# Optimization experiments

Measured on AMD Instinct MI355X. Metric: run time of the kernel, lower is better.

## Reference

```python
import jax, jax.numpy as jnp
import numpy as np

HID = 64      # RNN hidden size (fixed in source)
K = 3         # B-spline order (pykan default)
NUM = 5       # grid intervals (pykan default)
DIMS = [64, 16, 1]  # layer_nums_small_nobi


def make_grid(in_dim):
    # uniform grid on [-1,1] extended by K knots each side -> NUM+2K+1 = 12 knots
    h = 2.0 / NUM
    g = jnp.arange(-K, NUM + K + 1, dtype=jnp.float32) * h - 1.0
    return jnp.broadcast_to(g, (in_dim, g.shape[0]))


def bspline_basis(x, grid):
    # x: (b, in), grid: (in, G) -> basis (b, in, G-K-1) via Cox-de Boor
    xe = x[..., None]
    B = ((xe >= grid[:, :-1]) & (xe < grid[:, 1:])).astype(x.dtype)
    for d in range(1, K + 1):
        left = (xe - grid[:, :-(d + 1)]) / (grid[:, d:-1] - grid[:, :-(d + 1)]) * B[..., :-1]
        right = (grid[:, d + 1:] - xe) / (grid[:, d + 1:] - grid[:, 1:-d]) * B[..., 1:]
        B = left + right
    return B  # (b, in, NUM+K)


def kan_layer(x, grid, coef, sb, sp):
    # coef: (in, out, NUM+K); sb, sp: (in, out)
    bas = bspline_basis(x, grid)                      # (b, in, NUM+K)
    spl = jnp.einsum('bik,iok->bio', bas, coef)       # per-edge spline value
    return jnp.einsum('bi,io->bo', jax.nn.silu(x), sb) + jnp.einsum('bio,io->bo', spl, sp)


def rnn_layer(x, w_ih, w_hh, b_ih, b_hh, return_seq):
    # x: (b, t, f), tanh RNN, h0 = 0
    h0 = jnp.zeros((x.shape[0], HID), x.dtype)
    def step(h, xt):
        h = jnp.tanh(xt @ w_ih.T + h @ w_hh.T + b_ih + b_hh)
        return h, (h if return_seq else 0.0)
    hT, ys = jax.lax.scan(step, h0, jnp.swapaxes(x, 0, 1))
    return jnp.swapaxes(ys, 0, 1) if return_seq else hT


def setup_inputs() -> dict:
    key = jax.random.key(0)
    ks = jax.random.split(key, 16)
    Bsz, T, F = 2048, 256, 64
    s = 1.0 / np.sqrt(HID)
    inp = {'x': jax.random.normal(ks[0], (Bsz, T, F), jnp.float32)}
    inp['w_ih0'] = jax.random.uniform(ks[1], (HID, F), jnp.float32, -s, s)
    inp['w_hh0'] = jax.random.uniform(ks[2], (HID, HID), jnp.float32, -s, s)
    inp['b_ih0'] = jax.random.uniform(ks[3], (HID,), jnp.float32, -s, s)
    inp['b_hh0'] = jax.random.uniform(ks[4], (HID,), jnp.float32, -s, s)
    inp['w_ih1'] = jax.random.uniform(ks[5], (HID, HID), jnp.float32, -s, s)
    inp['w_hh1'] = jax.random.uniform(ks[6], (HID, HID), jnp.float32, -s, s)
    inp['b_ih1'] = jax.random.uniform(ks[7], (HID,), jnp.float32, -s, s)
    inp['b_hh1'] = jax.random.uniform(ks[8], (HID,), jnp.float32, -s, s)
    kk = 9
    for i, (di, do) in enumerate(zip(DIMS[:-1], DIMS[1:])):
        inp[f'grid{i}'] = make_grid(di)
        inp[f'coef{i}'] = 0.1 * jax.random.normal(ks[kk], (di, do, NUM + K), jnp.float32)
        inp[f'sb{i}'] = (1.0 / np.sqrt(di)) * jnp.ones((di, do), jnp.float32) + 0.05 * jax.random.normal(ks[kk + 1], (di, do), jnp.float32)
        inp[f'sp{i}'] = jnp.ones((di, do), jnp.float32)
        kk += 2
    return inp


def reference(x, w_ih0, w_hh0, b_ih0, b_hh0, w_ih1, w_hh1, b_ih1, b_hh1,
              grid0, coef0, sb0, sp0, grid1, coef1, sb1, sp1):
    h1 = rnn_layer(x, w_ih0, w_hh0, b_ih0, b_hh0, return_seq=True)   # (b,t,64)
    out = rnn_layer(h1, w_ih1, w_hh1, b_ih1, b_hh1, return_seq=False)  # last step only
    out = kan_layer(out, grid0, coef0, sb0, sp0)   # (b,16)
    out = kan_layer(out, grid1, coef1, sb1, sp1)   # (b,1)
    return jnp.squeeze(jax.nn.sigmoid(out), 1)     # (b,)
```

## Files before the change

kernel.cpp:

```cpp
#include <hip/hip_runtime.h>
#include <cstdint>
#include <cstddef>

typedef __attribute__((ext_vector_type(8))) __bf16 bf16x8;
typedef __attribute__((ext_vector_type(4))) float f32x4;

#define MFMA16(a, b, c) __builtin_amdgcn_mfma_f32_16x16x32_bf16((a), (b), (c), 0, 0, 0)

__device__ __forceinline__ float fast_tanh(float z) {
    float e = __expf(2.0f * z);
    return 1.0f - 2.0f * __builtin_amdgcn_rcpf(e + 1.0f);
}
__device__ __forceinline__ float fast_sigmoid(float z) {
    return __builtin_amdgcn_rcpf(1.0f + __expf(-z));
}

__device__ __forceinline__ unsigned pk2(float a, float b) {
    union { __bf16 h[2]; unsigned u; } p;
    p.h[0] = (__bf16)a;
    p.h[1] = (__bf16)b;
    return p.u;
}

__device__ __forceinline__ bf16x8 ldwfrag(const float* __restrict__ W, int row, int k0) {
    const float4 a = *(const float4*)(W + row * 64 + k0);
    const float4 b = *(const float4*)(W + row * 64 + k0 + 4);
    bf16x8 f;
    f[0] = (__bf16)a.x; f[1] = (__bf16)a.y; f[2] = (__bf16)a.z; f[3] = (__bf16)a.w;
    f[4] = (__bf16)b.x; f[5] = (__bf16)b.y; f[6] = (__bf16)b.z; f[7] = (__bf16)b.w;
    return f;
}

__device__ __forceinline__ void bspl8(float x, const float* kn, float* B) {
    float b[11];
#pragma unroll
    for (int m = 0; m < 11; ++m)
        b[m] = (x >= kn[m] && x < kn[m + 1]) ? 1.0f : 0.0f;
#pragma unroll
    for (int d = 1; d <= 3; ++d) {
#pragma unroll
        for (int m = 0; m + d < 11; ++m) {
            float lf = (x - kn[m]) / (kn[m + d] - kn[m]) * b[m];
            float rt = (kn[m + d + 1] - x) / (kn[m + d + 1] - kn[m + 1]) * b[m + 1];
            b[m] = lf + rt;
        }
    }
#pragma unroll
    for (int m = 0; m < 8; ++m) B[m] = b[m];
}

__global__ __launch_bounds__(256, 1) void rnn_kan_fused(
    const float* __restrict__ x,
    const float* __restrict__ wih0, const float* __restrict__ whh0,
    const float* __restrict__ bih0, const float* __restrict__ bhh0,
    const float* __restrict__ wih1, const float* __restrict__ whh1,
    const float* __restrict__ bih1, const float* __restrict__ bhh1,
    const float* __restrict__ grid0, const float* __restrict__ coef0,
    const float* __restrict__ sb0, const float* __restrict__ sp0,
    const float* __restrict__ grid1, const float* __restrict__ coef1,
    const float* __restrict__ sb1, const float* __restrict__ sp1,
    float* __restrict__ out)
{
    __shared__ __align__(16) float s_x[8][1024];
    __shared__ __align__(16) unsigned char s_h1[2][2048];
    __shared__ __align__(16) unsigned char s_h2[2][2048];
    __shared__ __align__(16) float s_hf[16][68];
    __shared__ __align__(16) float s_bas[1024][12];
    __shared__ __align__(16) float s_e[16][17];

    const int tid  = threadIdx.x;
    const int wv   = tid >> 6;
    const int lane = tid & 63;
    const int sc   = lane & 15;
    const int gr   = lane >> 4;
    const int s0   = blockIdx.x << 4;

    const int wrow = 16 * wv + sc;
    const int kofs = 8 * gr;
    bf16x8 fWih0[2], fWhh0[2], fWih1[2], fWhh1[2];
#pragma unroll
    for (int kt = 0; kt < 2; ++kt) {
        fWih0[kt] = ldwfrag(wih0, wrow, 32 * kt + kofs);
        fWhh0[kt] = ldwfrag(whh0, wrow, 32 * kt + kofs);
        fWih1[kt] = ldwfrag(wih1, wrow, 32 * kt + kofs);
        fWhh1[kt] = ldwfrag(whh1, wrow, 32 * kt + kofs);
    }
    f32x4 b0v, b1v, zv;
#pragma unroll
    for (int i = 0; i < 4; ++i) {
        const int h = 16 * wv + 4 * gr + i;
        b0v[i] = bih0[h] + bhh0[h];
        b1v[i] = bih1[h] + bhh1[h];
        zv[i] = 0.0f;
    }

    const int gs = 4 * wv + gr;
    const int gc = (lane & 15) ^ (gs & 7);
    const float* gsrc = x + (size_t)(s0 + gs) * 16384 + gc * 4;
    char* ldsx = (char*)(&s_x[0][0]);

    const unsigned swz  = (unsigned)(sc & 7) << 4;
    const unsigned offW  = sc * 128 + (((unsigned)(32 * wv + 8 * gr)) ^ swz);
    const unsigned offR0 = sc * 128 + (((unsigned)(16 * gr)) ^ swz);
    const unsigned offR1 = sc * 128 + (((unsigned)(64 + 16 * gr)) ^ swz);
    unsigned offX[4];
#pragma unroll
    for (int kt = 0; kt < 2; ++kt)
#pragma unroll
        for (int h = 0; h < 2; ++h)
            offX[2 * kt + h] = sc * 256 + 16 * ((unsigned)(8 * kt + 2 * gr + h) ^ (unsigned)(sc & 7));

    auto xw_compute = [&](int slot) -> f32x4 {
        const char* xb = (const char*)(&s_x[slot][0]);
        f32x4 acc = b0v;
#pragma unroll
        for (int kt = 0; kt < 2; ++kt) {
            const float4 q0 = *(const float4*)(xb + offX[2 * kt + 0]);
            const float4 q1 = *(const float4*)(xb + offX[2 * kt + 1]);
            bf16x8 xa;
            xa[0] = (__bf16)q0.x; xa[1] = (__bf16)q0.y; xa[2] = (__bf16)q0.z; xa[3] = (__bf16)q0.w;
            xa[4] = (__bf16)q1.x; xa[5] = (__bf16)q1.y; xa[6] = (__bf16)q1.z; xa[7] = (__bf16)q1.w;
            acc = MFMA16(fWih0[kt], xa, acc);
        }
        return acc;
    };

#pragma unroll
    for (int t = 0; t < 6; ++t) {
        __builtin_amdgcn_global_load_lds(
            (const __attribute__((address_space(1))) void*)(gsrc + t * 64),
            (__attribute__((address_space(3))) void*)(ldsx + t * 4096 + wv * 1024),
            16, 0, 0);
    }
    asm volatile("s_waitcnt vmcnt(3)" ::: "memory");
    __builtin_amdgcn_s_barrier();
    asm volatile("" ::: "memory");

    bf16x8 h1f[2], h2f[2];
    {
        bf16x8 zf;
#pragma unroll
        for (int e = 0; e < 8; ++e) zf[e] = (__bf16)0.0f;
        h1f[0] = zf; h1f[1] = zf; h2f[0] = zf; h2f[1] = zf;
    }

    f32x4 xw0 = xw_compute(0);
    f32x4 xw1 = xw_compute(1);

    for (int t = 0; t < 256; ++t) {
        const int par = t & 1;
        {
            const int ts = (t + 6 > 255) ? 255 : t + 6;
            __builtin_amdgcn_global_load_lds(
                (const __attribute__((address_space(1))) void*)(gsrc + ts * 64),
                (__attribute__((address_space(3))) void*)(ldsx + ((t + 6) & 7) * 4096 + wv * 1024),
                16, 0, 0);
        }
        f32x4 z1a = MFMA16(fWhh0[0], h1f[0], xw0);
        f32x4 z1b = MFMA16(fWhh0[1], h1f[1], zv);
        f32x4 z2a = MFMA16(fWih1[0], h1f[0], b1v);
        f32x4 z2b = MFMA16(fWih1[1], h1f[1], zv);
        f32x4 z2c = MFMA16(fWhh1[0], h2f[0], zv);
        f32x4 z2d = MFMA16(fWhh1[1], h2f[1], zv);

        f32x4 z1 = z1a + z1b;
        float v1[4];
#pragma unroll
        for (int i = 0; i < 4; ++i) v1[i] = fast_tanh(z1[i]);
        uint2 pw1; pw1.x = pk2(v1[0], v1[1]); pw1.y = pk2(v1[2], v1[3]);
        *(uint2*)((char*)(&s_h1[par][0]) + offW) = pw1;

        f32x4 z2 = (z2a + z2b) + (z2c + z2d);
        float v2[4];
#pragma unroll
        for (int i = 0; i < 4; ++i) v2[i] = fast_tanh(z2[i]);
        if (t > 0) {
            uint2 pw2; pw2.x = pk2(v2[0], v2[1]); pw2.y = pk2(v2[2], v2[3]);
            *(uint2*)((char*)(&s_h2[par][0]) + offW) = pw2;
        }

        asm volatile("s_waitcnt vmcnt(3) lgkmcnt(0)" ::: "memory");
        __builtin_amdgcn_s_barrier();
        asm volatile("" ::: "memory");

        h1f[0] = *(const bf16x8*)((const char*)(&s_h1[par][0]) + offR0);
        h1f[1] = *(const bf16x8*)((const char*)(&s_h1[par][0]) + offR1);
        if (t > 0) {
            h2f[0] = *(const bf16x8*)((const char*)(&s_h2[par][0]) + offR0);
            h2f[1] = *(const bf16x8*)((const char*)(&s_h2[par][0]) + offR1);
        }

        xw0 = xw1;
        xw1 = xw_compute((t + 2) & 7);
    }

    {
        f32x4 z2a = MFMA16(fWih1[0], h1f[0], b1v);
        f32x4 z2b = MFMA16(fWih1[1], h1f[1], zv);
        f32x4 z2c = MFMA16(fWhh1[0], h2f[0], zv);
        f32x4 z2d = MFMA16(fWhh1[1], h2f[1], zv);
        f32x4 z2 = (z2a + z2b) + (z2c + z2d);
        f32x4 hv;
#pragma unroll
        for (int i = 0; i < 4; ++i) hv[i] = fast_tanh(z2[i]);
        *(f32x4*)(&s_hf[sc][16 * wv + 4 * gr]) = hv;
    }
    __syncthreads();

    float kn0[12], kn1[12];
#pragma unroll
    for (int m = 0; m < 12; ++m) { kn0[m] = grid0[m]; kn1[m] = grid1[m]; }

    for (int q = tid; q < 1024; q += 256) {
        const int i = q >> 4, s = q & 15;
        const float v = s_hf[s][i];
        float B[8];
        bspl8(v, kn0, B);
        *(float4*)(&s_bas[q][0]) = make_float4(B[0], B[1], B[2], B[3]);
        *(float4*)(&s_bas[q][4]) = make_float4(B[4], B[5], B[6], B[7]);
        s_bas[q][8] = v * fast_sigmoid(v);
    }
    __syncthreads();

    {
        const int s = tid >> 4, o = tid & 15;
        float acc = 0.0f;
        for (int i = 0; i < 64; ++i) {
            const int q = (i << 4) + s;
            const float4 B0 = *(const float4*)(&s_bas[q][0]);
            const float4 B1 = *(const float4*)(&s_bas[q][4]);
            const float sil = s_bas[q][8];
            const float* cp = coef0 + i * 128 + o * 8;
            const float4 c0 = *(const float4*)cp;
            const float4 c1 = *(const float4*)(cp + 4);
            const float spl = B0.x * c0.x + B0.y * c0.y + B0.z * c0.z + B0.w * c0.w +
                              B1.x * c1.x + B1.y * c1.y + B1.z * c1.z + B1.w * c1.w;
            acc += sil * sb0[(i << 4) + o] + sp0[(i << 4) + o] * spl;
        }
        float B[8];
        bspl8(acc, kn1, B);
        const float* cp = coef1 + o * 8;
        float spl = 0.0f;
#pragma unroll
        for (int k = 0; k < 8; ++k) spl += B[k] * cp[k];
        s_e[s][o] = (acc * fast_sigmoid(acc)) * sb1[o] + sp1[o] * spl;
    }
    __syncthreads();

    if (tid < 16) {
        float sum = 0.0f;
#pragma unroll
        for (int o = 0; o < 16; ++o) sum += s_e[tid][o];
        out[s0 + tid] = fast_sigmoid(sum);
    }
}

extern "C" void kernel_launch(void* const* d_in, const int* in_sizes, int n_in,
                              void* d_out, int out_size, void* d_ws, size_t ws_size,
                              hipStream_t stream) {
    (void)n_in; (void)out_size; (void)d_ws; (void)ws_size;
    const int B = in_sizes[0] / (256 * 64);
    const int grid = B / 16;
    rnn_kan_fused<<<dim3(grid), dim3(256), 0, stream>>>(
        (const float*)d_in[0],
        (const float*)d_in[1], (const float*)d_in[2], (const float*)d_in[3], (const float*)d_in[4],
        (const float*)d_in[5], (const float*)d_in[6], (const float*)d_in[7], (const float*)d_in[8],
        (const float*)d_in[9], (const float*)d_in[10], (const float*)d_in[11], (const float*)d_in[12],
        (const float*)d_in[13], (const float*)d_in[14], (const float*)d_in[15], (const float*)d_in[16],
        (float*)d_out);
}
```

Before: 151.4 us.

## Load x directly to registers and restructure recurrence MFMA chains off critical path

Drops the LDS staging ring for x fed by global_load_lds and instead prefetches each step's input fragments straight from global memory into registers, three steps ahead. The per-step MFMAs become accumulator chains, and the h2 recurrent product (Whh1·h2) is computed after the barrier so it overlaps with the next step's work rather than sitting on the tanh critical path. This removes LDS traffic, one vmcnt wait and the zero-accumulator adds, at the cost of more registers and global loads that are less coalesced.

Measured after the change: 165.6 us. +9.4%, slower.

```diff
diff --git a/kernel.cpp b/kernel.cpp
--- a/kernel.cpp
+++ b/kernel.cpp
@@ -20,6 +20,13 @@
     p.h[0] = (__bf16)a;
     p.h[1] = (__bf16)b;
     return p.u;
+}
+
+__device__ __forceinline__ bf16x8 cvt8(float4 a, float4 b) {
+    bf16x8 f;
+    f[0] = (__bf16)a.x; f[1] = (__bf16)a.y; f[2] = (__bf16)a.z; f[3] = (__bf16)a.w;
+    f[4] = (__bf16)b.x; f[5] = (__bf16)b.y; f[6] = (__bf16)b.z; f[7] = (__bf16)b.w;
+    return f;
 }
 
 __device__ __forceinline__ bf16x8 ldwfrag(const float* __restrict__ W, int row, int k0) {
@@ -49,7 +56,7 @@
     for (int m = 0; m < 8; ++m) B[m] = b[m];
 }
 
-__global__ __launch_bounds__(256, 1) void rnn_kan_fused(
+__global__ __launch_bounds__(256, 1) void rnn_kan_v4(
     const float* __restrict__ x,
     const float* __restrict__ wih0, const float* __restrict__ whh0,
     const float* __restrict__ bih0, const float* __restrict__ bhh0,
@@ -61,7 +68,6 @@
     const float* __restrict__ sb1, const float* __restrict__ sp1,
     float* __restrict__ out)
 {
-    __shared__ __align__(16) float s_x[8][1024];
     __shared__ __align__(16) unsigned char s_h1[2][2048];
     __shared__ __align__(16) unsigned char s_h2[2][2048];
     __shared__ __align__(16) float s_hf[16][68];
@@ -85,121 +91,94 @@
         fWih1[kt] = ldwfrag(wih1, wrow, 32 * kt + kofs);
         fWhh1[kt] = ldwfrag(whh1, wrow, 32 * kt + kofs);
     }
-    f32x4 b0v, b1v, zv;
+    f32x4 b0v, b1v;
 #pragma unroll
     for (int i = 0; i < 4; ++i) {
         const int h = 16 * wv + 4 * gr + i;
         b0v[i] = bih0[h] + bhh0[h];
         b1v[i] = bih1[h] + bhh1[h];
-        zv[i] = 0.0f;
-    }
-
-    const int gs = 4 * wv + gr;
-    const int gc = (lane & 15) ^ (gs & 7);
-    const float* gsrc = x + (size_t)(s0 + gs) * 16384 + gc * 4;
-    char* ldsx = (char*)(&s_x[0][0]);
+    }
 
     const unsigned swz  = (unsigned)(sc & 7) << 4;
     const unsigned offW  = sc * 128 + (((unsigned)(32 * wv + 8 * gr)) ^ swz);
     const unsigned offR0 = sc * 128 + (((unsigned)(16 * gr)) ^ swz);
     const unsigned offR1 = sc * 128 + (((unsigned)(64 + 16 * gr)) ^ swz);
-    unsigned offX[4];
-#pragma unroll
-    for (int kt = 0; kt < 2; ++kt)
-#pragma unroll
-        for (int h = 0; h < 2; ++h)
-            offX[2 * kt + h] = sc * 256 + 16 * ((unsigned)(8 * kt + 2 * gr + h) ^ (unsigned)(sc & 7));
-
-    auto xw_compute = [&](int slot) -> f32x4 {
-        const char* xb = (const char*)(&s_x[slot][0]);
-        f32x4 acc = b0v;
-#pragma unroll
-        for (int kt = 0; kt < 2; ++kt) {
-            const float4 q0 = *(const float4*)(xb + offX[2 * kt + 0]);
-            const float4 q1 = *(const float4*)(xb + offX[2 * kt + 1]);
-            bf16x8 xa;
-            xa[0] = (__bf16)q0.x; xa[1] = (__bf16)q0.y; xa[2] = (__bf16)q0.z; xa[3] = (__bf16)q0.w;
-            xa[4] = (__bf16)q1.x; xa[5] = (__bf16)q1.y; xa[6] = (__bf16)q1.z; xa[7] = (__bf16)q1.w;
-            acc = MFMA16(fWih0[kt], xa, acc);
-        }
-        return acc;
-    };
-
-#pragma unroll
-    for (int t = 0; t < 6; ++t) {
-        __builtin_amdgcn_global_load_lds(
-            (const __attribute__((address_space(1))) void*)(gsrc + t * 64),
-            (__attribute__((address_space(3))) void*)(ldsx + t * 4096 + wv * 1024),
-            16, 0, 0);
-    }
-    asm volatile("s_waitcnt vmcnt(3)" ::: "memory");
+
+    const float* xb = x + (size_t)(s0 + sc) * 16384 + kofs;
+
+    float4 q0 = *(const float4*)(xb);      float4 q1 = *(const float4*)(xb + 4);
+    float4 q2 = *(const float4*)(xb + 32); float4 q3 = *(const float4*)(xb + 36);
+    float4 ra0 = *(const float4*)(xb + 64),  ra1 = *(const float4*)(xb + 68);
+    float4 ra2 = *(const float4*)(xb + 96),  ra3 = *(const float4*)(xb + 100);
+    float4 rb0 = *(const float4*)(xb + 128), rb1 = *(const float4*)(xb + 132);
+    float4 rb2 = *(const float4*)(xb + 160), rb3 = *(const float4*)(xb + 164);
+
+    f32x4 xz = MFMA16(fWih0[0], cvt8(q0, q1), b0v);
+    xz = MFMA16(fWih0[1], cvt8(q2, q3), xz);
+
+    {
+        float v[4];
+#pragma unroll
+        for (int i = 0; i < 4; ++i) v[i] = fast_tanh(xz[i]);
+        uint2 pw; pw.x = pk2(v[0], v[1]); pw.y = pk2(v[2], v[3]);
+        *(uint2*)((char*)(&s_h1[0][0]) + offW) = pw;
+    }
+    xz = MFMA16(fWih0[0], cvt8(ra0, ra1), b0v);
+    xz = MFMA16(fWih0[1], cvt8(ra2, ra3), xz);
+    ra0 = rb0; ra1 = rb1; ra2 = rb2; ra3 = rb3;
+    rb0 = *(const float4*)(xb + 192); rb1 = *(const float4*)(xb + 196);
+    rb2 = *(const float4*)(xb + 224); rb3 = *(const float4*)(xb + 228);
+
+    asm volatile("s_waitcnt lgkmcnt(0)" ::: "memory");
     __builtin_amdgcn_s_barrier();
     asm volatile("" ::: "memory");
 
-    bf16x8 h1f[2], h2f[2];
-    {
-        bf16x8 zf;
-#pragma unroll
-        for (int e = 0; e < 8; ++e) zf[e] = (__bf16)0.0f;
-        h1f[0] = zf; h1f[1] = zf; h2f[0] = zf; h2f[1] = zf;
-    }
-
-    f32x4 xw0 = xw_compute(0);
-    f32x4 xw1 = xw_compute(1);
-
-    for (int t = 0; t < 256; ++t) {
+    bf16x8 h1f0 = *(const bf16x8*)((const char*)(&s_h1[0][0]) + offR0);
+    bf16x8 h1f1 = *(const bf16x8*)((const char*)(&s_h1[0][0]) + offR1);
+    f32x4 h2z = b1v;
+
+    for (int t = 1; t < 256; ++t) {
         const int par = t & 1;
-        {
-            const int ts = (t + 6 > 255) ? 255 : t + 6;
-            __builtin_amdgcn_global_load_lds(
-                (const __attribute__((address_space(1))) void*)(gsrc + ts * 64),
-                (__attribute__((address_space(3))) void*)(ldsx + ((t + 6) & 7) * 4096 + wv * 1024),
-                16, 0, 0);
-        }
-        f32x4 z1a = MFMA16(fWhh0[0], h1f[0], xw0);
-        f32x4 z1b = MFMA16(fWhh0[1], h1f[1], zv);
-        f32x4 z2a = MFMA16(fWih1[0], h1f[0], b1v);
-        f32x4 z2b = MFMA16(fWih1[1], h1f[1], zv);
-        f32x4 z2c = MFMA16(fWhh1[0], h2f[0], zv);
-        f32x4 z2d = MFMA16(fWhh1[1], h2f[1], zv);
-
-        f32x4 z1 = z1a + z1b;
-        float v1[4];
+        f32x4 z1 = MFMA16(fWhh0[0], h1f0, xz);
+        z1 = MFMA16(fWhh0[1], h1f1, z1);
+        f32x4 z2 = MFMA16(fWih1[0], h1f0, h2z);
+        z2 = MFMA16(fWih1[1], h1f1, z2);
+
+        float v1[4], v2[4];
 #pragma unroll
         for (int i = 0; i < 4; ++i) v1[i] = fast_tanh(z1[i]);
         uint2 pw1; pw1.x = pk2(v1[0], v1[1]); pw1.y = pk2(v1[2], v1[3]);
         *(uint2*)((char*)(&s_h1[par][0]) + offW) = pw1;
-
-        f32x4 z2 = (z2a + z2b) + (z2c + z2d);
-        float v2[4];
 #pragma unroll
         for (int i = 0; i < 4; ++i) v2[i] = fast_tanh(z2[i]);
-        if (t > 0) {
-            uint2 pw2; pw2.x = pk2(v2[0], v2[1]); pw2.y = pk2(v2[2], v2[3]);
-            *(uint2*)((char*)(&s_h2[par][0]) + offW) = pw2;
+        uint2 pw2; pw2.x = pk2(v2[0], v2[1]); pw2.y = pk2(v2[2], v2[3]);
+        *(uint2*)((char*)(&s_h2[par][0]) + offW) = pw2;
+
+        xz = MFMA16(fWih0[0], cvt8(ra0, ra1), b0v);
+        xz = MFMA16(fWih0[1], cvt8(ra2, ra3), xz);
+        ra0 = rb0; ra1 = rb1; ra2 = rb2; ra3 = rb3;
+        {
+            const float* pn = xb + (size_t)((t + 3 > 255) ? 255 : t + 3) * 64;
+            rb0 = *(const float4*)(pn);      rb1 = *(const float4*)(pn + 4);
+            rb2 = *(const float4*)(pn + 32); rb3 = *(const float4*)(pn + 36);
         }
 
-        asm volatile("s_waitcnt vmcnt(3) lgkmcnt(0)" ::: "memory");
+        asm volatile("s_waitcnt lgkmcnt(0)" ::: "memory");
         __builtin_amdgcn_s_barrier();
         asm volatile("" ::: "memory");
 
-        h1f[0] = *(const bf16x8*)((const char*)(&s_h1[par][0]) + offR0);
-        h1f[1] = *(const bf16x8*)((const char*)(&s_h1[par][0]) + offR1);
-        if (t > 0) {
-            h2f[0] = *(const bf16x8*)((const char*)(&s_h2[par][0]) + offR0);
-            h2f[1] = *(const bf16x8*)((const char*)(&s_h2[par][0]) + offR1);
-        }
-
-        xw0 = xw1;
-        xw1 = xw_compute((t + 2) & 7);
+        bf16x8 h2f0 = *(const bf16x8*)((const char*)(&s_h2[par][0]) + offR0);
+        bf16x8 h2f1 = *(const bf16x8*)((const char*)(&s_h2[par][0]) + offR1);
+        h1f0 = *(const bf16x8*)((const char*)(&s_h1[par][0]) + offR0);
+        h1f1 = *(const bf16x8*)((const char*)(&s_h1[par][0]) + offR1);
+
+        h2z = MFMA16(fWhh1[0], h2f0, b1v);
+        h2z = MFMA16(fWhh1[1], h2f1, h2z);
     }
 
     {
-        f32x4 z2a = MFMA16(fWih1[0], h1f[0], b1v);
-        f32x4 z2b = MFMA16(fWih1[1], h1f[1], zv);
-        f32x4 z2c = MFMA16(fWhh1[0], h2f[0], zv);
-        f32x4 z2d = MFMA16(fWhh1[1], h2f[1], zv);
-        f32x4 z2 = (z2a + z2b) + (z2c + z2d);
+        f32x4 z2 = MFMA16(fWih1[0], h1f0, h2z);
+        z2 = MFMA16(fWih1[1], h1f1, z2);
         f32x4 hv;
 #pragma unroll
         for (int i = 0; i < 4; ++i) hv[i] = fast_tanh(z2[i]);
@@ -261,7 +240,7 @@
     (void)n_in; (void)out_size; (void)d_ws; (void)ws_size;
     const int B = in_sizes[0] / (256 * 64);
     const int grid = B / 16;
-    rnn_kan_fused<<<dim3(grid), dim3(256), 0, stream>>>(
+    rnn_kan_v4<<<dim3(grid), dim3(256), 0, stream>>>(
         (const float*)d_in[0],
         (const float*)d_in[1], (const float*)d_in[2], (const float*)d_in[3], (const float*)d_in[4],
         (const float*)d_in[5], (const float*)d_in[6], (const float*)d_in[7], (const float*)d_in[8],
```
